# Performance work log

Measured on AMD Instinct MI355X. Metric: run time of the kernel, lower is better.

The kernel has to match this reference:

```python
import jax, jax.numpy as jnp
import numpy as np

SEQ_LEN = 8192
HIDDEN = 1024
NUM_SPANS = 4096
MAX_W = 32  # max span width (end - start + 1 <= MAX_W)
NEG_INF = -1e9


def setup_inputs() -> dict:
    key = jax.random.key(0)
    k_emb, k_s, k_w, k_aw = jax.random.split(key, 4)
    embeddings = jax.random.normal(k_emb, (1, SEQ_LEN, HIDDEN), dtype=jnp.float32)
    starts = jax.random.randint(k_s, (NUM_SPANS,), 0, SEQ_LEN - MAX_W, dtype=jnp.int32)
    widths = jax.random.randint(k_w, (NUM_SPANS,), 0, MAX_W, dtype=jnp.int32)  # width-1 in [0, MAX_W-1]
    ends = starts + widths
    attn_w = jax.random.normal(k_aw, (HIDDEN,), dtype=jnp.float32) * (HIDDEN ** -0.5)
    attn_b = jnp.zeros((), dtype=jnp.float32)
    return {"embeddings": embeddings, "starts": starts, "ends": ends,
            "attn_w": attn_w, "attn_b": attn_b}


def reference(embeddings, starts, ends, attn_w, attn_b):
    emb = embeddings[0]  # (S_len, H) -- original code indexes batch 0
    # Padded span positions: (num_spans, MAX_W)
    pos = starts[:, None] + jnp.arange(MAX_W, dtype=starts.dtype)[None, :]
    mask = pos <= ends[:, None]
    pos_c = jnp.minimum(pos, SEQ_LEN - 1)
    span_emb = emb[pos_c]  # (num_spans, MAX_W, H) gather
    # Linear(H -> 1) attention scores, masked softmax over span positions
    scores = jnp.einsum("swh,h->sw", span_emb, attn_w) + attn_b
    scores = jnp.where(mask, scores, NEG_INF)
    weights = jax.nn.softmax(scores, axis=1)
    attn_out = jnp.einsum("sw,swh->sh", weights, span_emb)
    start_emb = emb[starts]  # (num_spans, H)
    end_emb = emb[ends]
    return jnp.concatenate([start_emb, end_emb, attn_out], axis=-1)  # (num_spans, 3H)
```

## Files before the change

kernel.cpp:

```cpp
#include <hip/hip_runtime.h>
#include <math.h>

#define SEQ_LEN   8192
#define HIDDEN    1024
#define NUM_SPANS 4096
#define MAX_W     32
#define NBLK2     2048
#define NXCD      8

typedef float f4v __attribute__((ext_vector_type(4)));

__device__ __forceinline__ float dot4(float4 a, float4 b) {
    return a.x * b.x + a.y * b.y + a.z * b.z + a.w * b.w;
}

__device__ __forceinline__ void nt_store4(float4* p, float4 v) {
    f4v x = { v.x, v.y, v.z, v.w };
    __builtin_nontemporal_store(x, (f4v*)p);
}

__global__ __launch_bounds__(1024) void prep_kernel(
    const int* __restrict__ starts,
    const float* __restrict__ emb,
    const float* __restrict__ attn_w,
    const float* __restrict__ attn_b,
    int* __restrict__ perm,
    float* __restrict__ scores)
{
    const int tid  = threadIdx.x;
    const int lane = tid & 63;
    const int wid  = tid >> 6;

    if (blockIdx.x != 0) {
        const int x = blockIdx.x & 7;
        const int k = (blockIdx.x >> 3) - (x == 0 ? 1 : 0);
        const int row = x * 1024 + k * 16 + wid;
        const float4* __restrict__ wv4 = (const float4*)attn_w;
        const float4 wv0 = wv4[lane];
        const float4 wv1 = wv4[lane + 64];
        const float4 wv2 = wv4[lane + 128];
        const float4 wv3 = wv4[lane + 192];
        const float4* __restrict__ rp = (const float4*)emb + (size_t)row * 256;
        float p = dot4(rp[lane],       wv0) + dot4(rp[lane + 64],  wv1)
                + dot4(rp[lane + 128], wv2) + dot4(rp[lane + 192], wv3);
        #pragma unroll
        for (int off = 32; off > 0; off >>= 1)
            p += __shfl_xor(p, off, 64);
        if (lane == 0) scores[row] = p + attn_b[0];
        return;
    }

    __shared__ int hist[1024];
    __shared__ int base[1024];
    __shared__ int wsum[16];

    hist[tid] = 0;
    __syncthreads();

    #pragma unroll
    for (int i = tid; i < NUM_SPANS; i += 1024)
        atomicAdd(&hist[starts[i] >> 3], 1);
    __syncthreads();

    const int v = hist[tid];
    int sc = v;
    #pragma unroll
    for (int off = 1; off < 64; off <<= 1) {
        const int t = __shfl_up(sc, off, 64);
        if (lane >= off) sc += t;
    }
    if (lane == 63) wsum[wid] = sc;
    __syncthreads();
    if (wid == 0 && lane < 16) {
        int ws = wsum[lane];
        #pragma unroll
        for (int off = 1; off < 16; off <<= 1) {
            const int t = __shfl_up(ws, off, 64);
            if (lane >= off) ws += t;
        }
        wsum[lane] = ws;
    }
    __syncthreads();
    const int waveOff = (wid == 0) ? 0 : wsum[wid - 1];
    base[tid] = waveOff + sc - v;
    __syncthreads();

    hist[tid] = 0;
    __syncthreads();

    #pragma unroll
    for (int i = tid; i < NUM_SPANS; i += 1024) {
        const int b   = starts[i] >> 3;
        const int pos = base[b] + atomicAdd(&hist[b], 1);
        perm[pos] = i;
    }
}

__global__ __launch_bounds__(256, 8) void span_repr_kernel(
    const float* __restrict__ emb,
    const int* __restrict__ starts,
    const int* __restrict__ ends,
    const int* __restrict__ perm,
    const float* __restrict__ scores,
    float* __restrict__ out)
{
    const int tid = threadIdx.x;
    const int w2  = tid >> 6;
    const int c   = tid & 63;

    const int slot = (blockIdx.x & (NXCD - 1)) * (NBLK2 / NXCD) + (blockIdx.x >> 3);
    const int s    = perm[(slot << 1) + (w2 >> 1)];
    const int h    = w2 & 1;

    const int start = starts[s];
    const int wmax  = ends[s] - start;

    const float sc = (c <= wmax) ? scores[start + c] : -INFINITY;
    float mx = sc;
    #pragma unroll
    for (int off = 32; off > 0; off >>= 1)
        mx = fmaxf(mx, __shfl_xor(mx, off, 64));
    const float e = (c <= wmax) ? __expf(sc - mx) : 0.0f;
    float sum = e;
    #pragma unroll
    for (int off = 32; off > 0; off >>= 1)
        sum += __shfl_xor(sum, off, 64);
    const float wt = e / sum;

    const float4* __restrict__ embr = (const float4*)emb + (size_t)start * 256 + (h << 7);
    float4* __restrict__ out4 = (float4*)(out + (size_t)s * (3 * HIDDEN)) + (h << 7);

    float4 v0 = embr[c];
    float4 v1 = embr[c + 64];
    nt_store4(&out4[c],      v0);
    nt_store4(&out4[c + 64], v1);

    const float w0 = __shfl(wt, 0, 64);
    float4 a0 = make_float4(w0 * v0.x, w0 * v0.y, w0 * v0.z, w0 * v0.w);
    float4 a1 = make_float4(w0 * v1.x, w0 * v1.y, w0 * v1.z, w0 * v1.w);

    const float4* nr = embr + (size_t)min(1, wmax) * 256;
    float4 p0 = nr[c];
    float4 p1 = nr[c + 64];

    for (int r = 1; r <= wmax; ++r) {
        const float4* __restrict__ xr = embr + (size_t)min(r + 1, wmax) * 256;
        float4 n0 = xr[c];
        float4 n1 = xr[c + 64];
        __builtin_amdgcn_sched_barrier(0);

        const float wr = __shfl(wt, r, 64);
        a0.x += wr * p0.x; a0.y += wr * p0.y; a0.z += wr * p0.z; a0.w += wr * p0.w;
        a1.x += wr * p1.x; a1.y += wr * p1.y; a1.z += wr * p1.z; a1.w += wr * p1.w;

        p0 = n0; p1 = n1;
    }

    nt_store4(&out4[256 + c],      p0);
    nt_store4(&out4[256 + c + 64], p1);

    nt_store4(&out4[512 + c],      a0);
    nt_store4(&out4[512 + c + 64], a1);
}

extern "C" void kernel_launch(void* const* d_in, const int* in_sizes, int n_in,
                              void* d_out, int out_size, void* d_ws, size_t ws_size,
                              hipStream_t stream) {
    const float* emb    = (const float*)d_in[0];
    const int*   starts = (const int*)d_in[1];
    const int*   ends   = (const int*)d_in[2];
    const float* attn_w = (const float*)d_in[3];
    const float* attn_b = (const float*)d_in[4];
    float* out = (float*)d_out;

    int*   perm   = (int*)d_ws;
    float* scores = (float*)((int*)d_ws + NUM_SPANS);

    prep_kernel<<<513, 1024, 0, stream>>>(starts, emb, attn_w, attn_b, perm, scores);
    span_repr_kernel<<<NBLK2, 256, 0, stream>>>(emb, starts, ends, perm, scores, out);
}
```

Before: 108.6 us.

## Process full-hidden spans per wave with block-aligned row walk for cache reuse

Each wave now computes one span over the full hidden dimension, and each block groups 8 consecutive sorted spans. Every wave iterates from a common aligned start row, giving zero weight to rows before its own start. This aims to make co-resident waves read the same embedding rows at the same time for cache reuse, and to halve per-span scheduling overhead. In exchange it adds extra zero-weight loads and iterations and raises per-lane register use.

```diff
diff --git a/kernel.cpp b/kernel.cpp
--- a/kernel.cpp
+++ b/kernel.cpp
@@ -5,7 +5,7 @@
 #define HIDDEN    1024
 #define NUM_SPANS 4096
 #define MAX_W     32
-#define NBLK2     2048
+#define NBLK3     512
 #define NXCD      8
 
 typedef float f4v __attribute__((ext_vector_type(4)));
@@ -96,7 +96,7 @@
     }
 }
 
-__global__ __launch_bounds__(256, 8) void span_repr_kernel(
+__global__ __launch_bounds__(512, 4) void span_repr_kernel(
     const float* __restrict__ emb,
     const int* __restrict__ starts,
     const int* __restrict__ ends,
@@ -105,15 +105,17 @@
     float* __restrict__ out)
 {
     const int tid = threadIdx.x;
-    const int w2  = tid >> 6;
+    const int wid = tid >> 6;
     const int c   = tid & 63;
 
-    const int slot = (blockIdx.x & (NXCD - 1)) * (NBLK2 / NXCD) + (blockIdx.x >> 3);
-    const int s    = perm[(slot << 1) + (w2 >> 1)];
-    const int h    = w2 & 1;
+    const int slot = (blockIdx.x & (NXCD - 1)) * (NBLK3 / NXCD) + (blockIdx.x >> 3);
+    const int s    = perm[(slot << 3) + wid];
 
     const int start = starts[s];
-    const int wmax  = ends[s] - start;
+    const int end   = ends[s];
+    const int wmax  = end - start;
+
+    const int t0 = starts[perm[slot << 3]] & ~7;
 
     const float sc = (c <= wmax) ? scores[start + c] : -INFINITY;
     float mx = sc;
@@ -127,40 +129,56 @@
         sum += __shfl_xor(sum, off, 64);
     const float wt = e / sum;
 
-    const float4* __restrict__ embr = (const float4*)emb + (size_t)start * 256 + (h << 7);
-    float4* __restrict__ out4 = (float4*)(out + (size_t)s * (3 * HIDDEN)) + (h << 7);
+    const float4* __restrict__ embr = (const float4*)emb;
+    float4* __restrict__ out4 = (float4*)(out + (size_t)s * (3 * HIDDEN));
 
-    float4 v0 = embr[c];
-    float4 v1 = embr[c + 64];
-    nt_store4(&out4[c],      v0);
-    nt_store4(&out4[c + 64], v1);
+    float4 a0 = make_float4(0.f, 0.f, 0.f, 0.f);
+    float4 a1 = make_float4(0.f, 0.f, 0.f, 0.f);
+    float4 a2 = make_float4(0.f, 0.f, 0.f, 0.f);
+    float4 a3 = make_float4(0.f, 0.f, 0.f, 0.f);
 
-    const float w0 = __shfl(wt, 0, 64);
-    float4 a0 = make_float4(w0 * v0.x, w0 * v0.y, w0 * v0.z, w0 * v0.w);
-    float4 a1 = make_float4(w0 * v1.x, w0 * v1.y, w0 * v1.z, w0 * v1.w);
+    const float4* rp = embr + (size_t)t0 * 256;
+    float4 v0 = rp[c];
+    float4 v1 = rp[c + 64];
+    float4 v2 = rp[c + 128];
+    float4 v3 = rp[c + 192];
 
-    const float4* nr = embr + (size_t)min(1, wmax) * 256;
-    float4 p0 = nr[c];
-    float4 p1 = nr[c + 64];
-
-    for (int r = 1; r <= wmax; ++r) {
-        const float4* __restrict__ xr = embr + (size_t)min(r + 1, wmax) * 256;
-        float4 n0 = xr[c];
-        float4 n1 = xr[c + 64];
+    for (int t = t0; t <= end; ++t) {
+        const float4* __restrict__ np = embr + (size_t)min(t + 1, end) * 256;
+        float4 n0 = np[c];
+        float4 n1 = np[c + 64];
+        float4 n2 = np[c + 128];
+        float4 n3 = np[c + 192];
         __builtin_amdgcn_sched_barrier(0);
 
-        const float wr = __shfl(wt, r, 64);
-        a0.x += wr * p0.x; a0.y += wr * p0.y; a0.z += wr * p0.z; a0.w += wr * p0.w;
-        a1.x += wr * p1.x; a1.y += wr * p1.y; a1.z += wr * p1.z; a1.w += wr * p1.w;
+        const int rr = t - start;
+        float wr = __shfl(wt, max(rr, 0), 64);
+        wr = (rr >= 0) ? wr : 0.0f;
 
-        p0 = n0; p1 = n1;
+        a0.x += wr * v0.x; a0.y += wr * v0.y; a0.z += wr * v0.z; a0.w += wr * v0.w;
+        a1.x += wr * v1.x; a1.y += wr * v1.y; a1.z += wr * v1.z; a1.w += wr * v1.w;
+        a2.x += wr * v2.x; a2.y += wr * v2.y; a2.z += wr * v2.z; a2.w += wr * v2.w;
+        a3.x += wr * v3.x; a3.y += wr * v3.y; a3.z += wr * v3.z; a3.w += wr * v3.w;
+
+        if (t == start) {
+            nt_store4(&out4[c],       v0);
+            nt_store4(&out4[c + 64],  v1);
+            nt_store4(&out4[c + 128], v2);
+            nt_store4(&out4[c + 192], v3);
+        }
+
+        v0 = n0; v1 = n1; v2 = n2; v3 = n3;
     }
 
-    nt_store4(&out4[256 + c],      p0);
-    nt_store4(&out4[256 + c + 64], p1);
+    nt_store4(&out4[256 + c],       v0);
+    nt_store4(&out4[256 + c + 64],  v1);
+    nt_store4(&out4[256 + c + 128], v2);
+    nt_store4(&out4[256 + c + 192], v3);
 
-    nt_store4(&out4[512 + c],      a0);
-    nt_store4(&out4[512 + c + 64], a1);
+    nt_store4(&out4[512 + c],       a0);
+    nt_store4(&out4[512 + c + 64],  a1);
+    nt_store4(&out4[512 + c + 128], a2);
+    nt_store4(&out4[512 + c + 192], a3);
 }
 
 extern "C" void kernel_launch(void* const* d_in, const int* in_sizes, int n_in,
@@ -177,5 +195,5 @@
     float* scores = (float*)((int*)d_ws + NUM_SPANS);
 
     prep_kernel<<<513, 1024, 0, stream>>>(starts, emb, attn_w, attn_b, perm, scores);
-    span_repr_kernel<<<NBLK2, 256, 0, stream>>>(emb, starts, ends, perm, scores, out);
+    span_repr_kernel<<<NBLK3, 512, 0, stream>>>(emb, starts, ends, perm, scores, out);
 }
```

Result: slower. 115.6 us (+6.4%).
